# Kernel optimization log

Hardware: AMD Instinct MI355X
Metric: run time of the kernel (lower is better)

Reference implementation:

```python
import jax, jax.numpy as jnp
import numpy as np
import math


def _cnot_perm(n, c, t):
    # permutation on basis states implementing CNOT(control=c, target=t), qubit 0 = MSB
    idx = np.arange(2 ** n)
    ctrl = (idx >> (n - 1 - c)) & 1
    return np.where(ctrl == 1, idx ^ (1 << (n - 1 - t)), idx)


def _rot(phi, theta, omega):
    # PennyLane Rot(phi, theta, omega) = RZ(omega) RY(theta) RZ(phi)
    c = jnp.cos(theta / 2.0)
    s = jnp.sin(theta / 2.0)
    m00 = jnp.exp(-0.5j * (phi + omega)) * c
    m01 = -jnp.exp(0.5j * (phi - omega)) * s
    m10 = jnp.exp(-0.5j * (phi - omega)) * s
    m11 = jnp.exp(0.5j * (phi + omega)) * c
    return jnp.stack([jnp.stack([m00, m01]), jnp.stack([m10, m11])])


def _apply_1q(state, U, q, n):
    # apply 2x2 gate U on qubit q of an [N, 2^n] statevector
    N = state.shape[0]
    s = state.reshape(N, 2 ** q, 2, 2 ** (n - q - 1))
    s = jnp.einsum('ab,nqbr->nqar', U, s)
    return s.reshape(N, 2 ** n)


def reference(x, weights, bias, filter_size, strides):
    fs, st = int(filter_size), int(strides)
    B, C, H, W = x.shape
    Cout, L, n, _ = weights.shape
    oh = (H - fs) // st + 1
    ow = (W - fs) // st + 1

    # im2col / torch.unfold: [B,C,oh,fs,ow,fs] -> [B,oh,ow,C,fs,fs] -> [N, C*fs*fs]
    rows = (jnp.arange(oh) * st)[:, None] + jnp.arange(fs)[None, :]
    cols = (jnp.arange(ow) * st)[:, None] + jnp.arange(fs)[None, :]
    patches = x[:, :, rows][:, :, :, :, cols]                 # [B,C,oh,fs,ow,fs]
    patches = patches.transpose(0, 2, 4, 1, 3, 5).reshape(B * oh * ow, C * fs * fs)

    D = C * fs * fs
    dim = 2 ** n
    if D < dim:
        patches = jnp.pad(patches, ((0, 0), (0, dim - D)))

    # amplitude-encoding normalization; all-zero patch vectors are masked to 0 output
    norm = jnp.linalg.norm(patches, axis=-1, keepdims=True)
    nonzero = (norm[:, 0] > 0).astype(patches.dtype)          # [N]
    state0 = (patches / jnp.where(norm > 0, norm, 1.0)).astype(jnp.complex64)

    perms = [jnp.asarray(_cnot_perm(n, q, (q + 1) % n)) for q in range(n)]
    sign = (1.0 - 2.0 * ((jnp.arange(dim) >> (n - 1)) & 1)).astype(jnp.float32)  # Z on qubit 0

    def run_channel(wc):  # wc: [L, n, 3]
        state = state0
        for l in range(L):
            for q in range(n):
                state = _apply_1q(state, _rot(wc[l, q, 0], wc[l, q, 1], wc[l, q, 2]), q, n)
            if n > 1:
                for q in range(n):  # CNOT ring
                    state = state[:, perms[q]]
        return jnp.sum((jnp.abs(state) ** 2) * sign, axis=-1)  # [N] expval Z0

    exps = jax.vmap(run_channel)(weights)                     # [Cout, N]
    out = exps * nonzero[None, :] + bias[:, None]
    return out.reshape(Cout, B, oh, ow).transpose(1, 0, 2, 3)


def setup_inputs() -> dict:
    key = jax.random.key(0)
    k1, k2, k3 = jax.random.split(key, 3)
    B, Cin, H, W = 32, 16, 64, 64
    Cout, L, fs, st = 8, 3, 4, 2
    D = Cin * fs * fs
    n = math.ceil(math.log2(D))
    x = jax.random.normal(k1, (B, Cin, H, W), dtype=jnp.float32)
    weights = jax.random.normal(k2, (Cout, L, n, 3), dtype=jnp.float32)
    kk = 1.0 / D
    bias = jax.random.uniform(k3, (Cout,), minval=-math.sqrt(kk), maxval=math.sqrt(kk), dtype=jnp.float32)
    return {"x": x, "weights": weights, "bias": bias, "filter_size": fs, "strides": st}
```

## Files before the change

kernel.cpp:

```cpp
#include <hip/hip_runtime.h>
#include <math.h>

#define NQ     8
#define DIM    256
#define LAYERS 3
#define COUT   8
#define NB     32
#define OH     31
#define OW     31
#define NPATCH (NB*OH*OW)
#define PT_BLK 512
#define NTILE  64
#define PTOT   (NTILE*PT_BLK)
#define NPTILE (PTOT/16)
#define NPAIR  72
#define MPACK  (NPAIR*64*8)

typedef _Float16 f16x8 __attribute__((ext_vector_type(8)));
typedef _Float16 f16x4 __attribute__((ext_vector_type(4)));
typedef _Float16 f16x2 __attribute__((ext_vector_type(2)));
typedef __fp16   h16x2 __attribute__((ext_vector_type(2)));
typedef float    f32x4 __attribute__((ext_vector_type(4)));

__device__ __forceinline__ float2 cmul(float2 a, float2 b) {
    return make_float2(a.x*b.x - a.y*b.y, a.x*b.y + a.y*b.x);
}
__device__ __forceinline__ float2 cadd(float2 a, float2 b) {
    return make_float2(a.x + b.x, a.y + b.y);
}

__device__ __forceinline__ int rho(int i) {
    #pragma unroll
    for (int q = 7; q >= 0; --q) {
        int t = (q + 1) & 7;
        if ((i >> (7 - q)) & 1) i ^= 1 << (7 - t);
    }
    return i;
}

__device__ __forceinline__ void gload_lds16(const _Float16* g, _Float16* l) {
    __builtin_amdgcn_global_load_lds(
        (const __attribute__((address_space(1))) void*)g,
        (__attribute__((address_space(3))) void*)l, 16, 0, 0);
}

__device__ __forceinline__ float fold4(f16x4 sv, f32x4 a, float o) {
    h16x2 s01 = __builtin_bit_cast(h16x2, (f16x2)__builtin_shufflevector(sv, sv, 0, 1));
    h16x2 s23 = __builtin_bit_cast(h16x2, (f16x2)__builtin_shufflevector(sv, sv, 2, 3));
    h16x2 y01 = __builtin_amdgcn_cvt_pkrtz(a[0], a[1]);
    h16x2 y23 = __builtin_amdgcn_cvt_pkrtz(a[2], a[3]);
    o = __builtin_amdgcn_fdot2(s01, y01, o, false);
    o = __builtin_amdgcn_fdot2(s23, y23, o, false);
    return o;
}

__device__ __forceinline__ float dpp_ror_add(float x, int ctrl) {
    int xi = __builtin_bit_cast(int, x);
    int yi;
    switch (ctrl) {
        case 0x128: yi = __builtin_amdgcn_update_dpp(0, xi, 0x128, 0xf, 0xf, true); break;
        case 0x124: yi = __builtin_amdgcn_update_dpp(0, xi, 0x124, 0xf, 0xf, true); break;
        case 0x122: yi = __builtin_amdgcn_update_dpp(0, xi, 0x122, 0xf, 0xf, true); break;
        default:    yi = __builtin_amdgcn_update_dpp(0, xi, 0x121, 0xf, 0xf, true); break;
    }
    return x + __builtin_bit_cast(float, yi);
}

__global__ __launch_bounds__(256) void wext(const float* __restrict__ w,
                                            _Float16* __restrict__ At,
                                            _Float16* __restrict__ Bt,
                                            const float* __restrict__ x,
                                            _Float16* __restrict__ sF) {
    __shared__ float2 g[96];
    __shared__ float2 vb[256];
    __shared__ _Float16 sT[16][264];
    __shared__ float rsums[16][4];

    if (blockIdx.x < 2048) {
        const int j  = blockIdx.x & 255;
        const int ch = blockIdx.x >> 8;
        const int i  = threadIdx.x;
        if (i < 24) {
            const float* wp = w + (ch*24 + i)*3;
            float phi = wp[0], th = wp[1], om = wp[2];
            float cth = cosf(th * 0.5f), sth = sinf(th * 0.5f);
            float a = 0.5f * (phi + om), b = 0.5f * (phi - om);
            float sa, ca, sb, cb;
            sincosf(a, &sa, &ca);
            sincosf(b, &sb, &cb);
            g[i*4+0] = make_float2( cth*ca, -cth*sa);
            g[i*4+1] = make_float2(-sth*cb, -sth*sb);
            g[i*4+2] = make_float2( sth*cb, -sth*sb);
            g[i*4+3] = make_float2( cth*ca,  cth*sa);
        }
        __syncthreads();

        float2 v = make_float2(1.f, 0.f);
        #pragma unroll
        for (int q = 0; q < 8; ++q) {
            int iq = (i >> (7 - q)) & 1, jq = (j >> (7 - q)) & 1;
            v = cmul(v, g[q*4 + iq*2 + jq]);
        }

        #pragma unroll
        for (int l = 1; l < 3; ++l) {
            vb[i] = v; __syncthreads();
            v = vb[rho(i)]; __syncthreads();
            #pragma unroll
            for (int q = 0; q < 2; ++q) {
                int bit = 1 << (7 - q);
                vb[i] = v; __syncthreads();
                float2 y = vb[i ^ bit]; __syncthreads();
                float2 m0 = (i & bit) ? g[(l*8+q)*4+3] : g[(l*8+q)*4+0];
                float2 m1 = (i & bit) ? g[(l*8+q)*4+2] : g[(l*8+q)*4+1];
                v = cadd(cmul(m0, v), cmul(m1, y));
            }
            #pragma unroll
            for (int q = 2; q < 8; ++q) {
                int bit = 1 << (7 - q);
                float2 y;
                y.x = __shfl_xor(v.x, bit, 64);
                y.y = __shfl_xor(v.y, bit, 64);
                float2 m0 = (i & bit) ? g[(l*8+q)*4+3] : g[(l*8+q)*4+0];
                float2 m1 = (i & bit) ? g[(l*8+q)*4+2] : g[(l*8+q)*4+1];
                v = cadd(cmul(m0, v), cmul(m1, y));
            }
        }
        vb[i] = v; __syncthreads();
        float2 a = vb[rho(i)];
        float sgn = (i & 128) ? -1.f : 1.f;
        size_t row = ((size_t)ch*256 + j) * 512;
        At[row + i]       = (_Float16)(sgn * a.x);
        At[row + 256 + i] = (_Float16)(sgn * a.y);
        Bt[row + i]       = (_Float16)a.x;
        Bt[row + 256 + i] = (_Float16)a.y;
    } else {
        const int tb  = blockIdx.x - 2048;
        const int tid = threadIdx.x;
        const int wv  = tid >> 6, lane = tid & 63;

        float2 va[4], vc[4];
        #pragma unroll
        for (int pp = 0; pp < 4; ++pp) {
            int pl = wv*4 + pp;
            int p  = tb*16 + pl;
            float2 v01 = make_float2(0.f,0.f), v23 = make_float2(0.f,0.f);
            if (p < NPATCH) {
                int b = p / (OH*OW); int r = p % (OH*OW);
                int oi = r / OW, oj = r % OW;
                int ci = lane >> 2, fi = lane & 3;
                const float* xb = x + (((size_t)(b*16 + ci))*64 + (oi*2 + fi))*64 + oj*2;
                v01 = *(const float2*)xb;
                v23 = *(const float2*)(xb + 2);
            }
            va[pp] = v01; vc[pp] = v23;
            float ss = v01.x*v01.x + v01.y*v01.y + v23.x*v23.x + v23.y*v23.y;
            ss = dpp_ror_add(ss, 0x128);
            ss = dpp_ror_add(ss, 0x124);
            ss = dpp_ror_add(ss, 0x122);
            ss = dpp_ror_add(ss, 0x121);
            if ((lane & 15) == 0) rsums[pl][lane >> 4] = ss;
        }
        __syncthreads();

        #pragma unroll
        for (int pp = 0; pp < 4; ++pp) {
            int pl = wv*4 + pp;
            float tot = rsums[pl][0] + rsums[pl][1] + rsums[pl][2] + rsums[pl][3];
            float inv = tot > 0.f ? 1.f / sqrtf(tot) : 0.f;
            f16x4 o;
            o[0] = (_Float16)(va[pp].x*inv); o[1] = (_Float16)(va[pp].y*inv);
            o[2] = (_Float16)(vc[pp].x*inv); o[3] = (_Float16)(vc[pp].y*inv);
            *(f16x4*)&sT[pl][lane*4] = o;
        }
        __syncthreads();

        #pragma unroll
        for (int e = 0; e < 2; ++e) {
            int vi = tid + e*256;
            int ks = vi >> 6, ln = vi & 63;
            int kq = ln >> 4, prow = ln & 15;
            f16x8 o = *(const f16x8*)&sT[prow][ks*32 + kq*8];
            ((f16x8*)sF)[(size_t)tb*512 + vi] = o;
        }
    }
}

__global__ __launch_bounds__(256) void build_Mp(const _Float16* __restrict__ At,
                                                const _Float16* __restrict__ Bt,
                                                _Float16* __restrict__ Mp) {
    const int ch = blockIdx.z;
    const int ti = blockIdx.y;
    const int wv = threadIdx.x >> 6;
    const int jt = blockIdx.x * 4 + wv;
    const int jt0 = 2 * (ti >> 1);
    if (jt < jt0) return;
    const int lane = threadIdx.x & 63;
    const int c16 = lane & 15, kq = lane >> 4;
    const int h = ti >> 1;
    const int offt = 8*ti - (h*(h-1) + h*(ti & 1));
    const int pidx = offt + (jt >> 1) - h;
    _Float16* Mc = Mp + (size_t)ch * MPACK;

    f32x4 acc = {0.f, 0.f, 0.f, 0.f};
    if (jt >= ti) {
        const _Float16* Ar = At + ((size_t)ch*256 + ti*16 + c16) * 512 + kq*8;
        const _Float16* Br = Bt + ((size_t)ch*256 + jt*16 + c16) * 512 + kq*8;
        #pragma unroll
        for (int kk = 0; kk < 16; ++kk) {
            f16x8 af = *(const f16x8*)(Ar + kk*32);
            f16x8 bf = *(const f16x8*)(Br + kk*32);
            acc = __builtin_amdgcn_mfma_f32_16x16x32_f16(af, bf, acc, 0, 0, 0);
        }
    }
    int wsel = (jt & 1) * 16 + c16;
    int kqp = wsel >> 3, jj = wsel & 7;
    #pragma unroll
    for (int reg = 0; reg < 4; ++reg) {
        int i_g = ti*16 + kq*4 + reg;
        int j_g = jt*16 + c16;
        float val = (jt >= ti) ? acc[reg] : 0.f;
        val *= (j_g > i_g) ? 2.f : ((j_g == i_g) ? 1.f : 0.f);
        Mc[(size_t)((pidx*64 + kqp*16 + (kq*4 + reg)) * 8 + jj)] = (_Float16)val;
    }
}

__global__ __attribute__((amdgpu_flat_work_group_size(512,512), amdgpu_waves_per_eu(2,4)))
void fusedqf(const _Float16* __restrict__ sF,
             const _Float16* __restrict__ Mp,
             const float* __restrict__ bias,
             float* __restrict__ out) {
    extern __shared__ _Float16 Mlds[];
    const int id   = blockIdx.x;
    const int xcd  = id & 7;
    const int g    = id >> 3;
    const int c    = g >> 3;
    const int tile = (g & 7) * 8 + xcd;
    const int tid  = threadIdx.x;
    const int lane = tid & 63;
    const int wv   = tid >> 6;
    const int prow = lane & 15, kq = lane >> 4;
    const int tp0  = tile*32 + wv*4;

    const _Float16* Msrc = Mp + (size_t)c * MPACK;
    #pragma unroll
    for (int it = 0; it < 9; ++it) {
        int off = (wv*9 + it) * 512;
        gload_lds16(Msrc + off + lane*8, Mlds + off);
    }

    f16x8 bfrag[4][4];
    #pragma unroll
    for (int pt = 0; pt < 4; ++pt) {
        const f16x8* src = (const f16x8*)sF + (size_t)(tp0 + pt)*512 + lane;
        #pragma unroll
        for (int ks = 0; ks < 4; ++ks)
            bfrag[pt][ks] = src[ks*64];
    }

    __syncthreads();

    const _Float16* fold0 = sF + ((size_t)tp0*512 + (kq>>1)*16 + prow)*8 + (kq&1)*4;
    float o0 = 0.f, o1 = 0.f, o2 = 0.f, o3 = 0.f;
    int pidx = 0;

    f16x4 svn[4];
    #pragma unroll
    for (int pt = 0; pt < 4; ++pt)
        svn[pt] = *(const f16x4*)(fold0 + pt*4096);

    #pragma unroll 1
    for (int t = 0; t < 8; ++t) {
        const int h = t >> 1;
        f16x4 svc[4];
        #pragma unroll
        for (int pt = 0; pt < 4; ++pt) svc[pt] = svn[pt];
        #pragma unroll
        for (int pt = 0; pt < 4; ++pt)
            svn[pt] = *(const f16x4*)(fold0 + pt*4096 + (t+1)*256);

        f32x4 a0 = {0,0,0,0}, a1 = {0,0,0,0}, a2 = {0,0,0,0}, a3 = {0,0,0,0};
        __builtin_amdgcn_s_setprio(1);
        #pragma unroll
        for (int ks = 0; ks < 4; ++ks) {
            if (ks >= h) {
                f16x8 m = *(const f16x8*)(Mlds + (size_t)pidx*512 + lane*8);
                a0 = __builtin_amdgcn_mfma_f32_16x16x32_f16(m, bfrag[0][ks], a0, 0, 0, 0);
                a1 = __builtin_amdgcn_mfma_f32_16x16x32_f16(m, bfrag[1][ks], a1, 0, 0, 0);
                a2 = __builtin_amdgcn_mfma_f32_16x16x32_f16(m, bfrag[2][ks], a2, 0, 0, 0);
                a3 = __builtin_amdgcn_mfma_f32_16x16x32_f16(m, bfrag[3][ks], a3, 0, 0, 0);
                ++pidx;
            }
        }
        __builtin_amdgcn_s_setprio(0);
        pidx += 4;

        o0 = fold4(svc[0], a0, o0);
        o1 = fold4(svc[1], a1, o1);
        o2 = fold4(svc[2], a2, o2);
        o3 = fold4(svc[3], a3, o3);
    }

    #pragma unroll
    for (int pt = 0; pt < 4; ++pt) {
        const f16x8* src = (const f16x8*)sF + (size_t)(tp0 + pt)*512 + lane;
        #pragma unroll
        for (int ks = 0; ks < 4; ++ks)
            bfrag[pt][ks] = src[(ks+4)*64];
    }

    pidx = 0;
    #pragma unroll
    for (int pt = 0; pt < 4; ++pt)
        svn[pt] = *(const f16x4*)(fold0 + pt*4096);

    #pragma unroll 1
    for (int t = 0; t < 16; ++t) {
        const int h = t >> 1;
        pidx += (h < 4) ? (4 - h) : 0;
        f16x4 svc[4];
        #pragma unroll
        for (int pt = 0; pt < 4; ++pt) svc[pt] = svn[pt];
        if (t < 15) {
            #pragma unroll
            for (int pt = 0; pt < 4; ++pt)
                svn[pt] = *(const f16x4*)(fold0 + pt*4096 + (t+1)*256);
        }

        f32x4 a0 = {0,0,0,0}, a1 = {0,0,0,0}, a2 = {0,0,0,0}, a3 = {0,0,0,0};
        __builtin_amdgcn_s_setprio(1);
        #pragma unroll
        for (int ks = 4; ks < 8; ++ks) {
            if (ks >= h) {
                f16x8 m = *(const f16x8*)(Mlds + (size_t)pidx*512 + lane*8);
                a0 = __builtin_amdgcn_mfma_f32_16x16x32_f16(m, bfrag[0][ks-4], a0, 0, 0, 0);
                a1 = __builtin_amdgcn_mfma_f32_16x16x32_f16(m, bfrag[1][ks-4], a1, 0, 0, 0);
                a2 = __builtin_amdgcn_mfma_f32_16x16x32_f16(m, bfrag[2][ks-4], a2, 0, 0, 0);
                a3 = __builtin_amdgcn_mfma_f32_16x16x32_f16(m, bfrag[3][ks-4], a3, 0, 0, 0);
                ++pidx;
            }
        }
        __builtin_amdgcn_s_setprio(0);

        o0 = fold4(svc[0], a0, o0);
        o1 = fold4(svc[1], a1, o1);
        o2 = fold4(svc[2], a2, o2);
        o3 = fold4(svc[3], a3, o3);
    }

    float ov[4] = {o0, o1, o2, o3};
    float bc = bias[c];
    #pragma unroll
    for (int pt = 0; pt < 4; ++pt) {
        float v = ov[pt];
        v += __shfl_xor(v, 16, 64);
        v += __shfl_xor(v, 32, 64);
        if (kq == 0) {
            int p = (tp0 + pt)*16 + prow;
            if (p < NPATCH) {
                int b = p / (OH*OW); int r2 = p % (OH*OW);
                int oi = r2 / OW, oj = r2 % OW;
                out[(((size_t)(b*COUT + c))*OH + oi)*OW + oj] = v + bc;
            }
        }
    }
}

extern "C" void kernel_launch(void* const* d_in, const int* in_sizes, int n_in,
                              void* d_out, int out_size, void* d_ws, size_t ws_size,
                              hipStream_t stream) {
    const float* x    = (const float*)d_in[0];
    const float* w    = (const float*)d_in[1];
    const float* bias = (const float*)d_in[2];
    float* out = (float*)d_out;

    const size_t OFF_AT  = 0;
    const size_t OFF_BT  = OFF_AT + 2097152;
    const size_t OFF_MP  = OFF_BT + 2097152;
    const size_t OFF_SF  = OFF_MP + 589824;
    const size_t TOTAL   = OFF_SF + 16777216;
    if (ws_size < TOTAL) return;

    char* ws = (char*)d_ws;
    _Float16* At = (_Float16*)(ws + OFF_AT);
    _Float16* Bt = (_Float16*)(ws + OFF_BT);
    _Float16* Mp = (_Float16*)(ws + OFF_MP);
    _Float16* sF = (_Float16*)(ws + OFF_SF);

    wext<<<2048 + NPTILE, 256, 0, stream>>>(w, At, Bt, x, sF);
    build_Mp<<<dim3(4, 16, COUT), 256, 0, stream>>>(At, Bt, Mp);
    fusedqf<<<NTILE*COUT, 512, MPACK*sizeof(_Float16), stream>>>(sF, Mp, bias, out);
}
```

Measured before the change: 54.09 us.

## Compute unitary columns per wavefront with register-held amplitudes, removing block barriers

```diff
diff --git a/kernel.cpp b/kernel.cpp
--- a/kernel.cpp
+++ b/kernel.cpp
@@ -15,6 +15,7 @@
 #define NPTILE (PTOT/16)
 #define NPAIR  72
 #define MPACK  (NPAIR*64*8)
+#define NWBLK  512
 
 typedef _Float16 f16x8 __attribute__((ext_vector_type(8)));
 typedef _Float16 f16x4 __attribute__((ext_vector_type(4)));
@@ -72,70 +73,111 @@
                                             const float* __restrict__ x,
                                             _Float16* __restrict__ sF) {
     __shared__ float2 g[96];
-    __shared__ float2 vb[256];
+    __shared__ float2 vb[1024];
     __shared__ _Float16 sT[16][264];
     __shared__ float rsums[16][4];
 
-    if (blockIdx.x < 2048) {
-        const int j  = blockIdx.x & 255;
-        const int ch = blockIdx.x >> 8;
-        const int i  = threadIdx.x;
-        if (i < 24) {
-            const float* wp = w + (ch*24 + i)*3;
+    if (blockIdx.x < NWBLK) {
+        const int ch  = blockIdx.x >> 6;
+        const int wv  = threadIdx.x >> 6;
+        const int l   = threadIdx.x & 63;
+        const int col = (blockIdx.x & 63) * 4 + wv;
+
+        if (threadIdx.x < 24) {
+            const float* wp = w + (ch*24 + threadIdx.x)*3;
             float phi = wp[0], th = wp[1], om = wp[2];
             float cth = cosf(th * 0.5f), sth = sinf(th * 0.5f);
             float a = 0.5f * (phi + om), b = 0.5f * (phi - om);
             float sa, ca, sb, cb;
             sincosf(a, &sa, &ca);
             sincosf(b, &sb, &cb);
-            g[i*4+0] = make_float2( cth*ca, -cth*sa);
-            g[i*4+1] = make_float2(-sth*cb, -sth*sb);
-            g[i*4+2] = make_float2( sth*cb, -sth*sb);
-            g[i*4+3] = make_float2( cth*ca,  cth*sa);
+            g[threadIdx.x*4+0] = make_float2( cth*ca, -cth*sa);
+            g[threadIdx.x*4+1] = make_float2(-sth*cb, -sth*sb);
+            g[threadIdx.x*4+2] = make_float2( sth*cb, -sth*sb);
+            g[threadIdx.x*4+3] = make_float2( cth*ca,  cth*sa);
         }
         __syncthreads();
 
-        float2 v = make_float2(1.f, 0.f);
-        #pragma unroll
-        for (int q = 0; q < 8; ++q) {
-            int iq = (i >> (7 - q)) & 1, jq = (j >> (7 - q)) & 1;
-            v = cmul(v, g[q*4 + iq*2 + jq]);
-        }
-
-        #pragma unroll
-        for (int l = 1; l < 3; ++l) {
-            vb[i] = v; __syncthreads();
-            v = vb[rho(i)]; __syncthreads();
+        float2* vcol = vb + wv * 256;
+        float2 v[4];
+        #pragma unroll
+        for (int k = 0; k < 4; ++k) {
+            int r = l + 64*k;
+            float2 acc = make_float2(1.f, 0.f);
             #pragma unroll
-            for (int q = 0; q < 2; ++q) {
-                int bit = 1 << (7 - q);
-                vb[i] = v; __syncthreads();
-                float2 y = vb[i ^ bit]; __syncthreads();
-                float2 m0 = (i & bit) ? g[(l*8+q)*4+3] : g[(l*8+q)*4+0];
-                float2 m1 = (i & bit) ? g[(l*8+q)*4+2] : g[(l*8+q)*4+1];
-                v = cadd(cmul(m0, v), cmul(m1, y));
+            for (int q = 0; q < 8; ++q) {
+                int iq = (r >> (7 - q)) & 1, jq = (col >> (7 - q)) & 1;
+                acc = cmul(acc, g[q*4 + iq*2 + jq]);
+            }
+            v[k] = acc;
+        }
+
+        #pragma unroll
+        for (int lay = 1; lay < 3; ++lay) {
+            #pragma unroll
+            for (int k = 0; k < 4; ++k) vcol[l + 64*k] = v[k];
+            #pragma unroll
+            for (int k = 0; k < 4; ++k) v[k] = vcol[rho(l + 64*k)];
+
+            {
+                const float2 g0 = g[(lay*8+0)*4+0], g1 = g[(lay*8+0)*4+1];
+                const float2 g2 = g[(lay*8+0)*4+2], g3 = g[(lay*8+0)*4+3];
+                float2 nv[4];
+                #pragma unroll
+                for (int k = 0; k < 4; ++k) {
+                    float2 xx = v[k], yy = v[k^2];
+                    nv[k] = (k & 2) ? cadd(cmul(g2, yy), cmul(g3, xx))
+                                    : cadd(cmul(g0, xx), cmul(g1, yy));
+                }
+                #pragma unroll
+                for (int k = 0; k < 4; ++k) v[k] = nv[k];
+            }
+            {
+                const float2 g0 = g[(lay*8+1)*4+0], g1 = g[(lay*8+1)*4+1];
+                const float2 g2 = g[(lay*8+1)*4+2], g3 = g[(lay*8+1)*4+3];
+                float2 nv[4];
+                #pragma unroll
+                for (int k = 0; k < 4; ++k) {
+                    float2 xx = v[k], yy = v[k^1];
+                    nv[k] = (k & 1) ? cadd(cmul(g2, yy), cmul(g3, xx))
+                                    : cadd(cmul(g0, xx), cmul(g1, yy));
+                }
+                #pragma unroll
+                for (int k = 0; k < 4; ++k) v[k] = nv[k];
             }
             #pragma unroll
             for (int q = 2; q < 8; ++q) {
                 int bit = 1 << (7 - q);
-                float2 y;
-                y.x = __shfl_xor(v.x, bit, 64);
-                y.y = __shfl_xor(v.y, bit, 64);
-                float2 m0 = (i & bit) ? g[(l*8+q)*4+3] : g[(l*8+q)*4+0];
-                float2 m1 = (i & bit) ? g[(l*8+q)*4+2] : g[(l*8+q)*4+1];
-                v = cadd(cmul(m0, v), cmul(m1, y));
-            }
-        }
-        vb[i] = v; __syncthreads();
-        float2 a = vb[rho(i)];
-        float sgn = (i & 128) ? -1.f : 1.f;
-        size_t row = ((size_t)ch*256 + j) * 512;
-        At[row + i]       = (_Float16)(sgn * a.x);
-        At[row + 256 + i] = (_Float16)(sgn * a.y);
-        Bt[row + i]       = (_Float16)a.x;
-        Bt[row + 256 + i] = (_Float16)a.y;
+                const float2 g0 = g[(lay*8+q)*4+0], g1 = g[(lay*8+q)*4+1];
+                const float2 g2 = g[(lay*8+q)*4+2], g3 = g[(lay*8+q)*4+3];
+                #pragma unroll
+                for (int k = 0; k < 4; ++k) {
+                    float2 yy;
+                    yy.x = __shfl_xor(v[k].x, bit, 64);
+                    yy.y = __shfl_xor(v[k].y, bit, 64);
+                    float2 m0 = (l & bit) ? g3 : g0;
+                    float2 m1 = (l & bit) ? g2 : g1;
+                    v[k] = cadd(cmul(m0, v[k]), cmul(m1, yy));
+                }
+            }
+        }
+        #pragma unroll
+        for (int k = 0; k < 4; ++k) vcol[l + 64*k] = v[k];
+        #pragma unroll
+        for (int k = 0; k < 4; ++k) v[k] = vcol[rho(l + 64*k)];
+
+        size_t rowb = ((size_t)ch*256 + col) * 512;
+        #pragma unroll
+        for (int k = 0; k < 4; ++k) {
+            int r = l + 64*k;
+            float sgn = (r & 128) ? -1.f : 1.f;
+            At[rowb + r]       = (_Float16)(sgn * v[k].x);
+            At[rowb + 256 + r] = (_Float16)(sgn * v[k].y);
+            Bt[rowb + r]       = (_Float16)v[k].x;
+            Bt[rowb + 256 + r] = (_Float16)v[k].y;
+        }
     } else {
-        const int tb  = blockIdx.x - 2048;
+        const int tb  = blockIdx.x - NWBLK;
         const int tid = threadIdx.x;
         const int wv  = tid >> 6, lane = tid & 63;
 
@@ -387,7 +429,7 @@
     _Float16* Mp = (_Float16*)(ws + OFF_MP);
     _Float16* sF = (_Float16*)(ws + OFF_SF);
 
-    wext<<<2048 + NPTILE, 256, 0, stream>>>(w, At, Bt, x, sF);
+    wext<<<NWBLK + NPTILE, 256, 0, stream>>>(w, At, Bt, x, sF);
     build_Mp<<<dim3(4, 16, COUT), 256, 0, stream>>>(At, Bt, Mp);
     fusedqf<<<NTILE*COUT, 512, MPACK*sizeof(_Float16), stream>>>(sF, Mp, bias, out);
 }
```

Result: faster. 52.35 us (-3.2%).
